# Optimization experiments

Hardware: AMD Instinct MI355X
Metric: run time of the kernel (lower is better)

The kernel has to match this reference:

```python
import jax, jax.numpy as jnp
import numpy as np

INPUT_SIZE = 7
HIDDEN = 64
OUT = 1
B, T = 2048, 512


def setup_inputs() -> dict:
    key = jax.random.key(0)
    ks = jax.random.split(key, 11)
    s_ih0 = 1.0 / np.sqrt(HIDDEN)
    def u(k, shape, s):
        return jax.random.uniform(k, shape, jnp.float32, -s, s)
    return {
        "x": jax.random.normal(ks[0], (B, T, INPUT_SIZE), jnp.float32),
        "W_ih0": u(ks[1], (3 * HIDDEN, INPUT_SIZE), s_ih0),
        "W_hh0": u(ks[2], (3 * HIDDEN, HIDDEN), s_ih0),
        "b_ih0": u(ks[3], (3 * HIDDEN,), s_ih0),
        "b_hh0": u(ks[4], (3 * HIDDEN,), s_ih0),
        "W_ih1": u(ks[5], (3 * HIDDEN, HIDDEN), s_ih0),
        "W_hh1": u(ks[6], (3 * HIDDEN, HIDDEN), s_ih0),
        "b_ih1": u(ks[7], (3 * HIDDEN,), s_ih0),
        "b_hh1": u(ks[8], (3 * HIDDEN,), s_ih0),
        "fc_W": u(ks[9], (OUT, HIDDEN), s_ih0),
        "fc_b": u(ks[10], (OUT,), s_ih0),
    }


def _gru_layer(x_seq, W_ih, W_hh, b_ih, b_hh):
    # x_seq: [B, T, D_in]; returns full hidden trajectory [B, T, H]
    Bsz = x_seq.shape[0]
    H = W_hh.shape[1]
    # precompute input-side gates for all timesteps (one big GEMM)
    xg = jnp.einsum('btd,gd->btg', x_seq, W_ih) + b_ih  # [B, T, 3H]

    def step(h, xg_t):
        hg = h @ W_hh.T + b_hh                     # [B, 3H]
        xr, xz, xn = jnp.split(xg_t, 3, axis=-1)
        hr, hz, hn = jnp.split(hg, 3, axis=-1)
        r = jax.nn.sigmoid(xr + hr)
        z = jax.nn.sigmoid(xz + hz)
        n = jnp.tanh(xn + r * hn)
        h_new = (1.0 - z) * n + z * h
        return h_new, h_new

    h0 = jnp.zeros((Bsz, H), x_seq.dtype)
    _, hs = jax.lax.scan(step, h0, jnp.swapaxes(xg, 0, 1))  # [T, B, H]
    return jnp.swapaxes(hs, 0, 1)


def reference(x, W_ih0, W_hh0, b_ih0, b_hh0, W_ih1, W_hh1, b_ih1, b_hh1, fc_W, fc_b):
    h1 = _gru_layer(x, W_ih0, W_hh0, b_ih0, b_hh0)   # [B, T, H]
    h2 = _gru_layer(h1, W_ih1, W_hh1, b_ih1, b_hh1)  # [B, T, H]
    last = h2[:, -1, :]                               # [B, H]
    return last @ fc_W.T + fc_b                       # [B, 1]
```

## Files before the change

### kernel.cpp

```cpp
#include <hip/hip_runtime.h>

#define NT 512
#define DIN 7
#define CTC 64
#define NBATCH 2048

typedef _Float16 half4 __attribute__((ext_vector_type(4)));
typedef _Float16 half8 __attribute__((ext_vector_type(8)));
typedef float    f32x4 __attribute__((ext_vector_type(4)));

#define MFMA32(A, B, C) __builtin_amdgcn_mfma_f32_16x16x32_f16((A), (B), (C), 0, 0, 0)

__device__ __forceinline__ float rcp_fast(float x) { return __builtin_amdgcn_rcpf(x); }
__device__ __forceinline__ float exp2_raw(float x) {
  float r;
  asm("v_exp_f32 %0, %1" : "=v"(r) : "v"(x));
  return r;
}
__device__ __forceinline__ float sigm2(float xs) { return rcp_fast(1.0f + exp2_raw(xs)); }
__device__ __forceinline__ float tanh2(float vs) {
  return fmaf(-2.0f, rcp_fast(1.0f + exp2_raw(vs)), 1.0f);
}

#define S_RZ (-1.4426950408889634f)
#define S_N  ( 2.8853900817779268f)

__global__ __launch_bounds__(512, 1) void gru8(
    const float* __restrict__ x,
    const float* __restrict__ Wih0,
    const float* __restrict__ Whh0,
    const float* __restrict__ bih0,
    const float* __restrict__ bhh0,
    const float* __restrict__ Wih1,
    const float* __restrict__ Whh1,
    const float* __restrict__ bih1,
    const float* __restrict__ bhh1,
    const float* __restrict__ fcW,
    const float* __restrict__ fcb,
    float* __restrict__ out)
{
  __shared__ __align__(16) _Float16 H0[2][8][16][8];
  __shared__ __align__(16) _Float16 H1[2][8][16][8];
  __shared__ __align__(16) _Float16 xb[16][CTC + 1][8];
  __shared__ float red[4][16];

  const int tid = threadIdx.x;
  const int col = tid & 15;
  const int q   = (tid >> 4) & 3;
  const int wv  = tid >> 6;
  const bool isL0 = (wv < 4);
  const int w   = wv & 3;
  const int s0  = blockIdx.x * 16;

  for (int i = tid; i < 2 * 8 * 16 * 8; i += 512) {
    ((_Float16*)H0)[i] = (_Float16)0; ((_Float16*)H1)[i] = (_Float16)0;
  }

  const int gr = w * 16 + col, gz = (4 + w) * 16 + col, gn = (8 + w) * 16 + col;
  const int bo = w * 16 + 4 * q;

  f32x4 bR, bZ, bXN, bHN;
  {
    const float* bi = isL0 ? bih0 : bih1;
    const float* bh = isL0 ? bhh0 : bhh1;
    f32x4 t1 = *(const f32x4*)&bi[bo],       t2 = *(const f32x4*)&bh[bo];
    bR = (t1 + t2) * S_RZ;
    t1 = *(const f32x4*)&bi[64 + bo];        t2 = *(const f32x4*)&bh[64 + bo];
    bZ = (t1 + t2) * S_RZ;
    bXN = *(const f32x4*)&bi[128 + bo] * S_N;
    bHN = *(const f32x4*)&bh[128 + bo] * S_N;
  }

  half8 Wa0 = {}, Wa1 = {}, Wa2 = {};
  half8 A0k0, A0k1, A1k0, A1k1, A2k0, A2k1;
  half8 B0k0 = {}, B0k1 = {}, B1k0 = {}, B1k1 = {}, B2k0 = {}, B2k1 = {};

#define LDW8(dst, W, g, kt, sc) do {                               \
    f32x4 _a = *(const f32x4*)&(W)[(g) * 64 + 32 * (kt) + 8 * q];  \
    f32x4 _b = *(const f32x4*)&(W)[(g) * 64 + 32 * (kt) + 8 * q + 4]; \
    half8 _h;                                                       \
    _h[0] = (_Float16)(_a[0] * (sc)); _h[1] = (_Float16)(_a[1] * (sc)); \
    _h[2] = (_Float16)(_a[2] * (sc)); _h[3] = (_Float16)(_a[3] * (sc)); \
    _h[4] = (_Float16)(_b[0] * (sc)); _h[5] = (_Float16)(_b[1] * (sc)); \
    _h[6] = (_Float16)(_b[2] * (sc)); _h[7] = (_Float16)(_b[3] * (sc)); \
    (dst) = _h;                                                     \
  } while (0)

  if (isL0) {
    if (q == 0) {
#pragma unroll
      for (int i = 0; i < DIN; ++i) {
        Wa0[i] = (_Float16)(Wih0[gr * DIN + i] * S_RZ);
        Wa1[i] = (_Float16)(Wih0[gz * DIN + i] * S_RZ);
        Wa2[i] = (_Float16)(Wih0[gn * DIN + i] * S_N);
      }
    }
    LDW8(A0k0, Whh0, gr, 0, S_RZ); LDW8(A0k1, Whh0, gr, 1, S_RZ);
    LDW8(A1k0, Whh0, gz, 0, S_RZ); LDW8(A1k1, Whh0, gz, 1, S_RZ);
    LDW8(A2k0, Whh0, gn, 0, S_N);  LDW8(A2k1, Whh0, gn, 1, S_N);
  } else {
    LDW8(A0k0, Wih1, gr, 0, S_RZ); LDW8(A0k1, Wih1, gr, 1, S_RZ);
    LDW8(A1k0, Wih1, gz, 0, S_RZ); LDW8(A1k1, Wih1, gz, 1, S_RZ);
    LDW8(A2k0, Wih1, gn, 0, S_N);  LDW8(A2k1, Wih1, gn, 1, S_N);
    LDW8(B0k0, Whh1, gr, 0, S_RZ); LDW8(B0k1, Whh1, gr, 1, S_RZ);
    LDW8(B1k0, Whh1, gz, 0, S_RZ); LDW8(B1k1, Whh1, gz, 1, S_RZ);
    LDW8(B2k0, Whh1, gn, 0, S_N);  LDW8(B2k1, Whh1, gn, 1, S_N);
  }
#undef LDW8
  __syncthreads();

  f32x4 hown = (f32x4){};
  const int woct = 2 * w + (q >> 1);
  const int woff = 4 * (q & 1);

  for (int k = 0; k <= NT; ++k) {
    const int p = k & 1;

    if ((k & (CTC - 1)) == 0 && k < NT) {
      for (int e = tid; e < 16 * CTC; e += 512) {
        const int ss = e & 15, tt = e >> 4;
        const float* xp = x + ((size_t)(s0 + ss) * NT + k + tt) * DIN;
        half8 v = (half8){};
#pragma unroll
        for (int d = 0; d < DIN; ++d) v[d] = (_Float16)xp[d];
        *(half8*)&xb[ss][tt][0] = v;
      }
      __syncthreads();
    }

    if (isL0) {
      if (k < NT) {
        const int ti = k & (CTC - 1);
        half8 hh0 = *(const half8*)&H0[p][q][col][0];
        half8 hh1 = *(const half8*)&H0[p][4 + q][col][0];
        half8 xf = *(const half8*)&xb[col][ti][0];

        f32x4 ar  = MFMA32(A0k0, hh0, MFMA32(Wa0, xf, bR));
        f32x4 ar2 = MFMA32(A0k1, hh1, (f32x4){});
        f32x4 az  = MFMA32(A1k0, hh0, MFMA32(Wa1, xf, bZ));
        f32x4 az2 = MFMA32(A1k1, hh1, (f32x4){});
        f32x4 axn = MFMA32(Wa2, xf, bXN);
        f32x4 ahn = MFMA32(A2k0, hh0, bHN);
        f32x4 ahn2 = MFMA32(A2k1, hh1, (f32x4){});
        ar += ar2; az += az2; ahn += ahn2;

        half4 nh;
#pragma unroll
        for (int i = 0; i < 4; ++i) {
          const float r = sigm2(ar[i]);
          const float z = sigm2(az[i]);
          const float n = tanh2(fmaf(r, ahn[i], axn[i]));
          hown[i] = fmaf(z, hown[i] - n, n);
          nh[i] = (_Float16)hown[i];
        }
        *(half4*)&H0[p ^ 1][woct][col][woff] = nh;
      }
    } else {
      if (k > 0) {
        half8 g0h0 = *(const half8*)&H0[p][q][col][0];
        half8 g0h1 = *(const half8*)&H0[p][4 + q][col][0];
        half8 g1h0 = *(const half8*)&H1[p ^ 1][q][col][0];
        half8 g1h1 = *(const half8*)&H1[p ^ 1][4 + q][col][0];

        f32x4 br  = MFMA32(A0k1, g0h1, MFMA32(A0k0, g0h0, bR));
        f32x4 br2 = MFMA32(B0k1, g1h1, MFMA32(B0k0, g1h0, (f32x4){}));
        f32x4 bz  = MFMA32(A1k1, g0h1, MFMA32(A1k0, g0h0, bZ));
        f32x4 bz2 = MFMA32(B1k1, g1h1, MFMA32(B1k0, g1h0, (f32x4){}));
        f32x4 bxn = MFMA32(A2k1, g0h1, MFMA32(A2k0, g0h0, bXN));
        f32x4 bhn = MFMA32(B2k1, g1h1, MFMA32(B2k0, g1h0, bHN));
        br += br2; bz += bz2;

        half4 nh;
#pragma unroll
        for (int i = 0; i < 4; ++i) {
          const float r = sigm2(br[i]);
          const float z = sigm2(bz[i]);
          const float n = tanh2(fmaf(r, bhn[i], bxn[i]));
          hown[i] = fmaf(z, hown[i] - n, n);
          nh[i] = (_Float16)hown[i];
        }
        *(half4*)&H1[p][woct][col][woff] = nh;
      }
    }
    __syncthreads();
  }

  if (!isL0) {
    f32x4 fw = *(const f32x4*)&fcW[bo];
    float partial = hown[0] * fw[0] + hown[1] * fw[1] +
                    hown[2] * fw[2] + hown[3] * fw[3];
    partial += __shfl_xor(partial, 16, 64);
    partial += __shfl_xor(partial, 32, 64);
    if ((tid & 63) < 16) red[w][col] = partial;
  }
  __syncthreads();
  if (tid < 16) {
    out[s0 + tid] = red[0][tid] + red[1][tid] + red[2][tid] + red[3][tid] + fcb[0];
  }
}

extern "C" void kernel_launch(void* const* d_in, const int* in_sizes, int n_in,
                              void* d_out, int out_size, void* d_ws, size_t ws_size,
                              hipStream_t stream) {
  (void)in_sizes; (void)n_in; (void)d_ws; (void)ws_size; (void)out_size;
  gru8<<<NBATCH / 16, 512, 0, stream>>>(
      (const float*)d_in[0],  (const float*)d_in[1],
      (const float*)d_in[2],  (const float*)d_in[3],
      (const float*)d_in[4],  (const float*)d_in[5],
      (const float*)d_in[6],  (const float*)d_in[7],
      (const float*)d_in[8],  (const float*)d_in[9],
      (const float*)d_in[10],
      (float*)d_out);
}
```

Measured before the change: 300.7 us.

## Restructure timestep loop into chunked nest with x prefetch, setprio and packed conversion

Splits the 513-step loop into chunks of 64 steps, with the x staging done at each chunk boundary. The last layer-1 step is peeled into an epilogue so the inner loop has no k<NT test. Layer 0 prefetches the next timestep's x fragment from LDS right after its MFMAs, which takes the LDS read off the critical path. MFMA blocks are wrapped in s_setprio to raise wave priority, and the fp16 packing uses cvt_pkrtz, which rounds toward zero instead of to nearest and slightly changes numerics.

After: 276.3 us. 1.09x faster.

```diff
diff --git a/kernel.cpp b/kernel.cpp
--- a/kernel.cpp
+++ b/kernel.cpp
@@ -3,6 +3,7 @@
 #define NT 512
 #define DIN 7
 #define CTC 64
+#define NCH (NT / CTC)
 #define NBATCH 2048
 
 typedef _Float16 half4 __attribute__((ext_vector_type(4)));
@@ -20,6 +21,13 @@
 __device__ __forceinline__ float sigm2(float xs) { return rcp_fast(1.0f + exp2_raw(xs)); }
 __device__ __forceinline__ float tanh2(float vs) {
   return fmaf(-2.0f, rcp_fast(1.0f + exp2_raw(vs)), 1.0f);
+}
+
+__device__ __forceinline__ half4 pack_h4(float a, float b, float c, float d) {
+  unsigned int lo = __builtin_bit_cast(unsigned int, __builtin_amdgcn_cvt_pkrtz(a, b));
+  unsigned int hi = __builtin_bit_cast(unsigned int, __builtin_amdgcn_cvt_pkrtz(c, d));
+  unsigned long long u = ((unsigned long long)hi << 32) | lo;
+  return __builtin_bit_cast(half4, u);
 }
 
 #define S_RZ (-1.4426950408889634f)
@@ -107,34 +115,35 @@
     LDW8(B2k0, Whh1, gn, 0, S_N);  LDW8(B2k1, Whh1, gn, 1, S_N);
   }
 #undef LDW8
-  __syncthreads();
 
   f32x4 hown = (f32x4){};
   const int woct = 2 * w + (q >> 1);
   const int woff = 4 * (q & 1);
 
-  for (int k = 0; k <= NT; ++k) {
-    const int p = k & 1;
-
-    if ((k & (CTC - 1)) == 0 && k < NT) {
-      for (int e = tid; e < 16 * CTC; e += 512) {
-        const int ss = e & 15, tt = e >> 4;
-        const float* xp = x + ((size_t)(s0 + ss) * NT + k + tt) * DIN;
-        half8 v = (half8){};
+  half8 xf_pref = (half8){};
+
+  for (int m = 0; m < NCH; ++m) {
+    __syncthreads();
+    for (int e = tid; e < 16 * CTC; e += 512) {
+      const int ss = e & 15, tt = e >> 4;
+      const float* xp = x + ((size_t)(s0 + ss) * NT + m * CTC + tt) * DIN;
+      half8 v = (half8){};
 #pragma unroll
-        for (int d = 0; d < DIN; ++d) v[d] = (_Float16)xp[d];
-        *(half8*)&xb[ss][tt][0] = v;
-      }
-      __syncthreads();
-    }
-
-    if (isL0) {
-      if (k < NT) {
-        const int ti = k & (CTC - 1);
+      for (int d = 0; d < DIN; ++d) v[d] = (_Float16)xp[d];
+      *(half8*)&xb[ss][tt][0] = v;
+    }
+    __syncthreads();
+
+    for (int ti = 0; ti < CTC; ++ti) {
+      const int k = m * CTC + ti;
+      const int p = ti & 1;
+
+      if (isL0) {
         half8 hh0 = *(const half8*)&H0[p][q][col][0];
         half8 hh1 = *(const half8*)&H0[p][4 + q][col][0];
-        half8 xf = *(const half8*)&xb[col][ti][0];
-
+        half8 xf = (ti == 0) ? *(const half8*)&xb[col][0][0] : xf_pref;
+
+        __builtin_amdgcn_s_setprio(1);
         f32x4 ar  = MFMA32(A0k0, hh0, MFMA32(Wa0, xf, bR));
         f32x4 ar2 = MFMA32(A0k1, hh1, (f32x4){});
         f32x4 az  = MFMA32(A1k0, hh0, MFMA32(Wa1, xf, bZ));
@@ -142,50 +151,89 @@
         f32x4 axn = MFMA32(Wa2, xf, bXN);
         f32x4 ahn = MFMA32(A2k0, hh0, bHN);
         f32x4 ahn2 = MFMA32(A2k1, hh1, (f32x4){});
+        __builtin_amdgcn_s_setprio(0);
+
+        xf_pref = *(const half8*)&xb[col][ti + 1][0];
+
         ar += ar2; az += az2; ahn += ahn2;
-
-        half4 nh;
+        float h0c, h1c, h2c, h3c;
+        {
+          const float r0 = sigm2(ar[0]), z0 = sigm2(az[0]);
+          const float n0 = tanh2(fmaf(r0, ahn[0], axn[0]));
+          h0c = fmaf(z0, hown[0] - n0, n0);
+          const float r1 = sigm2(ar[1]), z1 = sigm2(az[1]);
+          const float n1 = tanh2(fmaf(r1, ahn[1], axn[1]));
+          h1c = fmaf(z1, hown[1] - n1, n1);
+          const float r2 = sigm2(ar[2]), z2 = sigm2(az[2]);
+          const float n2 = tanh2(fmaf(r2, ahn[2], axn[2]));
+          h2c = fmaf(z2, hown[2] - n2, n2);
+          const float r3 = sigm2(ar[3]), z3 = sigm2(az[3]);
+          const float n3 = tanh2(fmaf(r3, ahn[3], axn[3]));
+          h3c = fmaf(z3, hown[3] - n3, n3);
+        }
+        hown[0] = h0c; hown[1] = h1c; hown[2] = h2c; hown[3] = h3c;
+        *(half4*)&H0[p ^ 1][woct][col][woff] = pack_h4(h0c, h1c, h2c, h3c);
+      } else {
+        if (k > 0) {
+          half8 g0h0 = *(const half8*)&H0[p][q][col][0];
+          half8 g0h1 = *(const half8*)&H0[p][4 + q][col][0];
+          half8 g1h0 = *(const half8*)&H1[p ^ 1][q][col][0];
+          half8 g1h1 = *(const half8*)&H1[p ^ 1][4 + q][col][0];
+
+          __builtin_amdgcn_s_setprio(1);
+          f32x4 br  = MFMA32(A0k1, g0h1, MFMA32(A0k0, g0h0, bR));
+          f32x4 br2 = MFMA32(B0k1, g1h1, MFMA32(B0k0, g1h0, (f32x4){}));
+          f32x4 bz  = MFMA32(A1k1, g0h1, MFMA32(A1k0, g0h0, bZ));
+          f32x4 bz2 = MFMA32(B1k1, g1h1, MFMA32(B1k0, g1h0, (f32x4){}));
+          f32x4 bxn = MFMA32(A2k1, g0h1, MFMA32(A2k0, g0h0, bXN));
+          f32x4 bhn = MFMA32(B2k1, g1h1, MFMA32(B2k0, g1h0, bHN));
+          __builtin_amdgcn_s_setprio(0);
+          br += br2; bz += bz2;
+
+          float h0c, h1c, h2c, h3c;
+          {
+            const float r0 = sigm2(br[0]), z0 = sigm2(bz[0]);
+            const float n0 = tanh2(fmaf(r0, bhn[0], bxn[0]));
+            h0c = fmaf(z0, hown[0] - n0, n0);
+            const float r1 = sigm2(br[1]), z1 = sigm2(bz[1]);
+            const float n1 = tanh2(fmaf(r1, bhn[1], bxn[1]));
+            h1c = fmaf(z1, hown[1] - n1, n1);
+            const float r2 = sigm2(br[2]), z2 = sigm2(bz[2]);
+            const float n2 = tanh2(fmaf(r2, bhn[2], bxn[2]));
+            h2c = fmaf(z2, hown[2] - n2, n2);
+            const float r3 = sigm2(br[3]), z3 = sigm2(bz[3]);
+            const float n3 = tanh2(fmaf(r3, bhn[3], bxn[3]));
+            h3c = fmaf(z3, hown[3] - n3, n3);
+          }
+          hown[0] = h0c; hown[1] = h1c; hown[2] = h2c; hown[3] = h3c;
+          *(half4*)&H1[p][woct][col][woff] = pack_h4(h0c, h1c, h2c, h3c);
+        }
+      }
+      __syncthreads();
+    }
+  }
+
+  if (!isL0) {
+    half8 g0h0 = *(const half8*)&H0[0][q][col][0];
+    half8 g0h1 = *(const half8*)&H0[0][4 + q][col][0];
+    half8 g1h0 = *(const half8*)&H1[1][q][col][0];
+    half8 g1h1 = *(const half8*)&H1[1][4 + q][col][0];
+
+    f32x4 br  = MFMA32(A0k1, g0h1, MFMA32(A0k0, g0h0, bR));
+    f32x4 br2 = MFMA32(B0k1, g1h1, MFMA32(B0k0, g1h0, (f32x4){}));
+    f32x4 bz  = MFMA32(A1k1, g0h1, MFMA32(A1k0, g0h0, bZ));
+    f32x4 bz2 = MFMA32(B1k1, g1h1, MFMA32(B1k0, g1h0, (f32x4){}));
+    f32x4 bxn = MFMA32(A2k1, g0h1, MFMA32(A2k0, g0h0, bXN));
+    f32x4 bhn = MFMA32(B2k1, g1h1, MFMA32(B2k0, g1h0, bHN));
+    br += br2; bz += bz2;
+
 #pragma unroll
-        for (int i = 0; i < 4; ++i) {
-          const float r = sigm2(ar[i]);
-          const float z = sigm2(az[i]);
-          const float n = tanh2(fmaf(r, ahn[i], axn[i]));
-          hown[i] = fmaf(z, hown[i] - n, n);
-          nh[i] = (_Float16)hown[i];
-        }
-        *(half4*)&H0[p ^ 1][woct][col][woff] = nh;
-      }
-    } else {
-      if (k > 0) {
-        half8 g0h0 = *(const half8*)&H0[p][q][col][0];
-        half8 g0h1 = *(const half8*)&H0[p][4 + q][col][0];
-        half8 g1h0 = *(const half8*)&H1[p ^ 1][q][col][0];
-        half8 g1h1 = *(const half8*)&H1[p ^ 1][4 + q][col][0];
-
-        f32x4 br  = MFMA32(A0k1, g0h1, MFMA32(A0k0, g0h0, bR));
-        f32x4 br2 = MFMA32(B0k1, g1h1, MFMA32(B0k0, g1h0, (f32x4){}));
-        f32x4 bz  = MFMA32(A1k1, g0h1, MFMA32(A1k0, g0h0, bZ));
-        f32x4 bz2 = MFMA32(B1k1, g1h1, MFMA32(B1k0, g1h0, (f32x4){}));
-        f32x4 bxn = MFMA32(A2k1, g0h1, MFMA32(A2k0, g0h0, bXN));
-        f32x4 bhn = MFMA32(B2k1, g1h1, MFMA32(B2k0, g1h0, bHN));
-        br += br2; bz += bz2;
-
-        half4 nh;
-#pragma unroll
-        for (int i = 0; i < 4; ++i) {
-          const float r = sigm2(br[i]);
-          const float z = sigm2(bz[i]);
-          const float n = tanh2(fmaf(r, bhn[i], bxn[i]));
-          hown[i] = fmaf(z, hown[i] - n, n);
-          nh[i] = (_Float16)hown[i];
-        }
-        *(half4*)&H1[p][woct][col][woff] = nh;
-      }
-    }
-    __syncthreads();
-  }
-
-  if (!isL0) {
+    for (int i = 0; i < 4; ++i) {
+      const float r = sigm2(br[i]);
+      const float z = sigm2(bz[i]);
+      const float n = tanh2(fmaf(r, bhn[i], bxn[i]));
+      hown[i] = fmaf(z, hown[i] - n, n);
+    }
     f32x4 fw = *(const f32x4*)&fcW[bo];
     float partial = hown[0] * fw[0] + hown[1] * fw[1] +
                     hown[2] * fw[2] + hown[3] * fw[3];
```

## Restructure GRU timestep loop into chunked, 2x-unrolled ticks with prefetch and priority hints

Applied to the files above, without the earlier changes.

The single timestep loop with per-step branch checks becomes a nested chunk loop unrolled by two, with static ping-pong buffer indices. The next input vector is prefetched from LDS while gate math runs, MFMA sections get s_setprio hints, and fp16 packing uses cvt_pkrtz. The final layer-1 step is peeled out of the loop and the redundant initial barrier is removed. This targets loop and branch overhead and LDS latency on the serial critical path. The cost is round-toward-zero instead of round-to-nearest when storing fp16 hidden state.

After: 269.9 us. -10.3%, faster.

```diff
diff --git a/kernel.cpp b/kernel.cpp
--- a/kernel.cpp
+++ b/kernel.cpp
@@ -3,6 +3,7 @@
 #define NT 512
 #define DIN 7
 #define CTC 64
+#define NCH (NT / CTC)
 #define NBATCH 2048
 
 typedef _Float16 half4 __attribute__((ext_vector_type(4)));
@@ -20,6 +21,13 @@
 __device__ __forceinline__ float sigm2(float xs) { return rcp_fast(1.0f + exp2_raw(xs)); }
 __device__ __forceinline__ float tanh2(float vs) {
   return fmaf(-2.0f, rcp_fast(1.0f + exp2_raw(vs)), 1.0f);
+}
+
+__device__ __forceinline__ half4 pack_h4(float a, float b, float c, float d) {
+  unsigned int lo = __builtin_bit_cast(unsigned int, __builtin_amdgcn_cvt_pkrtz(a, b));
+  unsigned int hi = __builtin_bit_cast(unsigned int, __builtin_amdgcn_cvt_pkrtz(c, d));
+  unsigned long long u = ((unsigned long long)hi << 32) | lo;
+  return __builtin_bit_cast(half4, u);
 }
 
 #define S_RZ (-1.4426950408889634f)
@@ -107,85 +115,124 @@
     LDW8(B2k0, Whh1, gn, 0, S_N);  LDW8(B2k1, Whh1, gn, 1, S_N);
   }
 #undef LDW8
-  __syncthreads();
 
   f32x4 hown = (f32x4){};
   const int woct = 2 * w + (q >> 1);
   const int woff = 4 * (q & 1);
 
-  for (int k = 0; k <= NT; ++k) {
-    const int p = k & 1;
-
-    if ((k & (CTC - 1)) == 0 && k < NT) {
-      for (int e = tid; e < 16 * CTC; e += 512) {
-        const int ss = e & 15, tt = e >> 4;
-        const float* xp = x + ((size_t)(s0 + ss) * NT + k + tt) * DIN;
-        half8 v = (half8){};
+#define L0_TICK(P, XFCUR, XFNXT, TIN) do {                                    \
+    half8 hh0 = *(const half8*)&H0[P][q][col][0];                             \
+    half8 hh1 = *(const half8*)&H0[P][4 + q][col][0];                         \
+    __builtin_amdgcn_s_setprio(1);                                            \
+    f32x4 ar  = MFMA32(A0k0, hh0, MFMA32(Wa0, XFCUR, bR));                    \
+    f32x4 ar2 = MFMA32(A0k1, hh1, (f32x4){});                                 \
+    f32x4 az  = MFMA32(A1k0, hh0, MFMA32(Wa1, XFCUR, bZ));                    \
+    f32x4 az2 = MFMA32(A1k1, hh1, (f32x4){});                                 \
+    f32x4 axn = MFMA32(Wa2, XFCUR, bXN);                                      \
+    f32x4 ahn = MFMA32(A2k0, hh0, bHN);                                       \
+    f32x4 ahn2 = MFMA32(A2k1, hh1, (f32x4){});                                \
+    __builtin_amdgcn_s_setprio(0);                                            \
+    XFNXT = *(const half8*)&xb[col][(TIN) + 1][0];                            \
+    ar += ar2; az += az2; ahn += ahn2;                                        \
+    const float r0 = sigm2(ar[0]), z0 = sigm2(az[0]);                         \
+    const float n0 = tanh2(fmaf(r0, ahn[0], axn[0]));                         \
+    const float h0c = fmaf(z0, hown[0] - n0, n0);                             \
+    const float r1 = sigm2(ar[1]), z1 = sigm2(az[1]);                         \
+    const float n1 = tanh2(fmaf(r1, ahn[1], axn[1]));                         \
+    const float h1c = fmaf(z1, hown[1] - n1, n1);                             \
+    const float r2 = sigm2(ar[2]), z2 = sigm2(az[2]);                         \
+    const float n2 = tanh2(fmaf(r2, ahn[2], axn[2]));                         \
+    const float h2c = fmaf(z2, hown[2] - n2, n2);                             \
+    const float r3 = sigm2(ar[3]), z3 = sigm2(az[3]);                         \
+    const float n3 = tanh2(fmaf(r3, ahn[3], axn[3]));                         \
+    const float h3c = fmaf(z3, hown[3] - n3, n3);                             \
+    hown[0] = h0c; hown[1] = h1c; hown[2] = h2c; hown[3] = h3c;               \
+    *(half4*)&H0[(P) ^ 1][woct][col][woff] = pack_h4(h0c, h1c, h2c, h3c);     \
+  } while (0)
+
+#define L1_TICK(P) do {                                                       \
+    half8 g0h0 = *(const half8*)&H0[P][q][col][0];                            \
+    half8 g0h1 = *(const half8*)&H0[P][4 + q][col][0];                        \
+    half8 g1h0 = *(const half8*)&H1[(P) ^ 1][q][col][0];                      \
+    half8 g1h1 = *(const half8*)&H1[(P) ^ 1][4 + q][col][0];                  \
+    __builtin_amdgcn_s_setprio(1);                                            \
+    f32x4 br  = MFMA32(A0k1, g0h1, MFMA32(A0k0, g0h0, bR));                   \
+    f32x4 br2 = MFMA32(B0k1, g1h1, MFMA32(B0k0, g1h0, (f32x4){}));            \
+    f32x4 bz  = MFMA32(A1k1, g0h1, MFMA32(A1k0, g0h0, bZ));                   \
+    f32x4 bz2 = MFMA32(B1k1, g1h1, MFMA32(B1k0, g1h0, (f32x4){}));            \
+    f32x4 bxn = MFMA32(A2k1, g0h1, MFMA32(A2k0, g0h0, bXN));                  \
+    f32x4 bhn = MFMA32(B2k1, g1h1, MFMA32(B2k0, g1h0, bHN));                  \
+    __builtin_amdgcn_s_setprio(0);                                            \
+    br += br2; bz += bz2;                                                     \
+    const float r0 = sigm2(br[0]), z0 = sigm2(bz[0]);                         \
+    const float n0 = tanh2(fmaf(r0, bhn[0], bxn[0]));                         \
+    const float h0c = fmaf(z0, hown[0] - n0, n0);                             \
+    const float r1 = sigm2(br[1]), z1 = sigm2(bz[1]);                         \
+    const float n1 = tanh2(fmaf(r1, bhn[1], bxn[1]));                         \
+    const float h1c = fmaf(z1, hown[1] - n1, n1);                             \
+    const float r2 = sigm2(br[2]), z2 = sigm2(bz[2]);                         \
+    const float n2 = tanh2(fmaf(r2, bhn[2], bxn[2]));                         \
+    const float h2c = fmaf(z2, hown[2] - n2, n2);                             \
+    const float r3 = sigm2(br[3]), z3 = sigm2(bz[3]);                         \
+    const float n3 = tanh2(fmaf(r3, bhn[3], bxn[3]));                         \
+    const float h3c = fmaf(z3, hown[3] - n3, n3);                             \
+    hown[0] = h0c; hown[1] = h1c; hown[2] = h2c; hown[3] = h3c;               \
+    *(half4*)&H1[P][woct][col][woff] = pack_h4(h0c, h1c, h2c, h3c);           \
+  } while (0)
+
+  for (int m = 0; m < NCH; ++m) {
+    for (int e = tid; e < 16 * CTC; e += 512) {
+      const int ss = e & 15, tt = e >> 4;
+      const float* xp = x + ((size_t)(s0 + ss) * NT + m * CTC + tt) * DIN;
+      half8 v = (half8){};
 #pragma unroll
-        for (int d = 0; d < DIN; ++d) v[d] = (_Float16)xp[d];
-        *(half8*)&xb[ss][tt][0] = v;
+      for (int d = 0; d < DIN; ++d) v[d] = (_Float16)xp[d];
+      *(half8*)&xb[ss][tt][0] = v;
+    }
+    __syncthreads();
+
+    half8 xfA = (half8){}, xfB = (half8){};
+    if (isL0) xfA = *(const half8*)&xb[col][0][0];
+
+    for (int th = 0; th < CTC; th += 2) {
+      if (isL0) {
+        L0_TICK(0, xfA, xfB, th);
+      } else if (m + th > 0) {
+        L1_TICK(0);
       }
       __syncthreads();
-    }
-
-    if (isL0) {
-      if (k < NT) {
-        const int ti = k & (CTC - 1);
-        half8 hh0 = *(const half8*)&H0[p][q][col][0];
-        half8 hh1 = *(const half8*)&H0[p][4 + q][col][0];
-        half8 xf = *(const half8*)&xb[col][ti][0];
-
-        f32x4 ar  = MFMA32(A0k0, hh0, MFMA32(Wa0, xf, bR));
-        f32x4 ar2 = MFMA32(A0k1, hh1, (f32x4){});
-        f32x4 az  = MFMA32(A1k0, hh0, MFMA32(Wa1, xf, bZ));
-        f32x4 az2 = MFMA32(A1k1, hh1, (f32x4){});
-        f32x4 axn = MFMA32(Wa2, xf, bXN);
-        f32x4 ahn = MFMA32(A2k0, hh0, bHN);
-        f32x4 ahn2 = MFMA32(A2k1, hh1, (f32x4){});
-        ar += ar2; az += az2; ahn += ahn2;
-
-        half4 nh;
+      if (isL0) {
+        L0_TICK(1, xfB, xfA, th + 1);
+      } else {
+        L1_TICK(1);
+      }
+      __syncthreads();
+    }
+  }
+#undef L0_TICK
+#undef L1_TICK
+
+  if (!isL0) {
+    half8 g0h0 = *(const half8*)&H0[0][q][col][0];
+    half8 g0h1 = *(const half8*)&H0[0][4 + q][col][0];
+    half8 g1h0 = *(const half8*)&H1[1][q][col][0];
+    half8 g1h1 = *(const half8*)&H1[1][4 + q][col][0];
+
+    f32x4 br  = MFMA32(A0k1, g0h1, MFMA32(A0k0, g0h0, bR));
+    f32x4 br2 = MFMA32(B0k1, g1h1, MFMA32(B0k0, g1h0, (f32x4){}));
+    f32x4 bz  = MFMA32(A1k1, g0h1, MFMA32(A1k0, g0h0, bZ));
+    f32x4 bz2 = MFMA32(B1k1, g1h1, MFMA32(B1k0, g1h0, (f32x4){}));
+    f32x4 bxn = MFMA32(A2k1, g0h1, MFMA32(A2k0, g0h0, bXN));
+    f32x4 bhn = MFMA32(B2k1, g1h1, MFMA32(B2k0, g1h0, bHN));
+    br += br2; bz += bz2;
+
 #pragma unroll
-        for (int i = 0; i < 4; ++i) {
-          const float r = sigm2(ar[i]);
-          const float z = sigm2(az[i]);
-          const float n = tanh2(fmaf(r, ahn[i], axn[i]));
-          hown[i] = fmaf(z, hown[i] - n, n);
-          nh[i] = (_Float16)hown[i];
-        }
-        *(half4*)&H0[p ^ 1][woct][col][woff] = nh;
-      }
-    } else {
-      if (k > 0) {
-        half8 g0h0 = *(const half8*)&H0[p][q][col][0];
-        half8 g0h1 = *(const half8*)&H0[p][4 + q][col][0];
-        half8 g1h0 = *(const half8*)&H1[p ^ 1][q][col][0];
-        half8 g1h1 = *(const half8*)&H1[p ^ 1][4 + q][col][0];
-
-        f32x4 br  = MFMA32(A0k1, g0h1, MFMA32(A0k0, g0h0, bR));
-        f32x4 br2 = MFMA32(B0k1, g1h1, MFMA32(B0k0, g1h0, (f32x4){}));
-        f32x4 bz  = MFMA32(A1k1, g0h1, MFMA32(A1k0, g0h0, bZ));
-        f32x4 bz2 = MFMA32(B1k1, g1h1, MFMA32(B1k0, g1h0, (f32x4){}));
-        f32x4 bxn = MFMA32(A2k1, g0h1, MFMA32(A2k0, g0h0, bXN));
-        f32x4 bhn = MFMA32(B2k1, g1h1, MFMA32(B2k0, g1h0, bHN));
-        br += br2; bz += bz2;
-
-        half4 nh;
-#pragma unroll
-        for (int i = 0; i < 4; ++i) {
-          const float r = sigm2(br[i]);
-          const float z = sigm2(bz[i]);
-          const float n = tanh2(fmaf(r, bhn[i], bxn[i]));
-          hown[i] = fmaf(z, hown[i] - n, n);
-          nh[i] = (_Float16)hown[i];
-        }
-        *(half4*)&H1[p][woct][col][woff] = nh;
-      }
-    }
-    __syncthreads();
-  }
-
-  if (!isL0) {
+    for (int i = 0; i < 4; ++i) {
+      const float r = sigm2(br[i]);
+      const float z = sigm2(bz[i]);
+      const float n = tanh2(fmaf(r, bhn[i], bxn[i]));
+      hown[i] = fmaf(z, hown[i] - n, n);
+    }
     f32x4 fw = *(const f32x4*)&fcW[bo];
     float partial = hown[0] * fw[0] + hown[1] * fw[1] +
                     hown[2] * fw[2] + hown[3] * fw[3];
```
